# Performance work log

Measured on AMD Instinct MI355X. Metric: run time of the kernel, lower is better.

## Reference

```python
import jax, jax.numpy as jnp
import numpy as np

KEY_DIM = 64
SCALE_PER_SEQ = 1.0 / np.sqrt(KEY_DIM).astype(np.float32)
SCALE_OVER_SEQS = 1.0 / np.sqrt(KEY_DIM).astype(np.float32)


def setup_inputs() -> dict:
    key = jax.random.key(0)
    ks = jax.random.split(key, 6)
    b, i, t, j, d, dv, kd = 4, 512, 32, 256, 512, 512, KEY_DIM
    w_scale = 0.05
    return {
        "input_seq": jax.random.normal(ks[0], (b, i, d), jnp.float32),
        "memory_x": jax.random.normal(ks[1], (b, t, j, d), jnp.float32),
        "memory_y": jax.random.normal(ks[2], (b, t, j, dv), jnp.float32),
        "Wq": jax.random.normal(ks[3], (d, kd), jnp.float32) * w_scale,
        "bq": jnp.zeros((kd,), jnp.float32),
        "Wk": jax.random.normal(ks[4], (d, kd), jnp.float32) * w_scale,
        "bk": jnp.zeros((kd,), jnp.float32),
        "Wv": jax.random.normal(ks[5], (dv, dv), jnp.float32) * w_scale,
        "bv": jnp.zeros((dv,), jnp.float32),
    }


def reference(input_seq, memory_x, memory_y, Wq, bq, Wk, bk, Wv, bv):
    # Projections (Dense layers)
    queries = input_seq @ Wq + bq          # [b, i, kd]
    keys = memory_x @ Wk + bk              # [b, t, j, kd]
    values = memory_y @ Wv + bv            # [b, t, j, dv]

    # Level 1: within-sequence attention
    attn_mat = jnp.einsum('bik,btjk->btij', queries, keys)          # [b, t, i, j]
    per_seq_attn = jax.nn.softmax(SCALE_PER_SEQ * attn_mat, axis=-1)
    per_seq_retrieved = jnp.einsum('btij,btjk->btik', per_seq_attn, values)  # [b, t, i, dv]

    # Level 2: over-sequences attention (max-reduce over j, softmax over t)
    mem_seq_attn = jnp.max(attn_mat, axis=-1)                       # [b, t, i]
    mem_seq_attn = jax.nn.softmax(SCALE_OVER_SEQS * mem_seq_attn, axis=1)

    retrieved = jnp.einsum('bti,btik->bik', mem_seq_attn, per_seq_retrieved)  # [b, i, dv]
    return retrieved
```

## Files before the change

kernel.cpp:

```cpp
#include <hip/hip_runtime.h>
#include <cstdint>

#define B_ 4
#define I_ 512
#define T_ 32
#define J_ 256
#define D_ 512
#define DV_ 512
#define KD_ 64
#define TJ_ (T_*J_)
#define BI_ (B_*I_)
#define MK_ (B_*T_*J_)

typedef unsigned short u16;
typedef __attribute__((ext_vector_type(8))) u16 u16x8;
typedef __attribute__((ext_vector_type(4))) u16 u16x4;
typedef __attribute__((ext_vector_type(8))) short bf16x8;
typedef __attribute__((ext_vector_type(4))) float f32x4;

__device__ __forceinline__ u16 f2bf(float f){
  unsigned u = __float_as_uint(f);
  u += 0x7fffu + ((u >> 16) & 1u);
  return (u16)(u >> 16);
}
__device__ __forceinline__ float bf2f(u16 h){ return __uint_as_float(((unsigned)h) << 16); }

#define GLD16(gsrc, ldst) __builtin_amdgcn_global_load_lds( \
    (const __attribute__((address_space(1))) unsigned int*)(gsrc), \
    (__attribute__((address_space(3))) unsigned int*)(ldst), 16, 0, 0)

__global__ __launch_bounds__(256) void k_prep(const float* __restrict__ Y, u16* __restrict__ Yt,
                                              const float* __restrict__ Wq, const float* __restrict__ Wk,
                                              const float* __restrict__ Wv, u16* __restrict__ wqt,
                                              u16* __restrict__ wkt, u16* __restrict__ wvt){
  __shared__ __align__(16) u16 tileT[64][72];
  int bid = blockIdx.x;
  int tid = threadIdx.x;
  if (bid < 4096){
    int kx = bid & 127, ny = (bid >> 7) & 7, b = bid >> 10;
    int k0 = kx*64, n0 = ny*64;
    #pragma unroll
    for (int s=0;s<4;++s){
      int idx = tid + s*256; int r = idx>>4, c4 = idx&15;
      const float4 v = *(const float4*)&Y[((size_t)b*TJ_ + k0 + r)*DV_ + n0 + c4*4];
      tileT[c4*4+0][r] = f2bf(v.x);
      tileT[c4*4+1][r] = f2bf(v.y);
      tileT[c4*4+2][r] = f2bf(v.z);
      tileT[c4*4+3][r] = f2bf(v.w);
    }
    __syncthreads();
    #pragma unroll
    for (int s=0;s<2;++s){
      int idx = tid + s*256; int rn = idx>>3, c8 = idx&7;
      *(u16x8*)&Yt[((size_t)b*DV_ + n0 + rn)*TJ_ + k0 + c8*8] = *(const u16x8*)&tileT[rn][c8*8];
    }
  } else {
    int gid = (bid - 4096)*256 + tid;
    if (gid < 32768){
      int n = gid >> 9, k = gid & 511;
      wqt[gid] = f2bf(Wq[(size_t)k*64 + n]);
    } else if (gid < 65536){
      int g = gid - 32768;
      int n = g >> 9, k = g & 511;
      wkt[g] = f2bf(Wk[(size_t)k*64 + n]);
    } else {
      int g = gid - 65536;
      int n = g >> 9, k = g & 511;
      wvt[g] = f2bf(Wv[(size_t)k*512 + n]);
    }
  }
}

__global__ __launch_bounds__(256) void k_proj(const float* __restrict__ mx, const float* __restrict__ iseq,
                                              const u16* __restrict__ wkt, const u16* __restrict__ wqt,
                                              const float* __restrict__ bk, const float* __restrict__ bq,
                                              u16* __restrict__ kbf, u16* __restrict__ qbf){
  __shared__ __align__(16) u16 As[32][72];
  __shared__ __align__(16) u16 Bs[64][72];
  int bid = blockIdx.x;
  const float* A; const u16* Bt; const float* bias; u16* C; int row0;
  if (bid < 1024){ A = mx;   Bt = wkt; bias = bk; C = kbf; row0 = bid*32; }
  else           { A = iseq; Bt = wqt; bias = bq; C = qbf; row0 = (bid-1024)*32; }
  int tid = threadIdx.x;
  int lane = tid & 63, wv = tid >> 6;
  int lrow = lane & 15, lk8 = (lane >> 4) * 8;
  int mf = wv >> 1, nfb = (wv & 1) * 2;
  int ar = tid >> 4, ac4 = tid & 15;
  int br = tid >> 3, bc8 = tid & 7;
  f32x4 acc[2];
  acc[0] = (f32x4){0.f,0.f,0.f,0.f}; acc[1] = (f32x4){0.f,0.f,0.f,0.f};

  float4 fa[2][2]; u16x8 fb[2][2];
  #define PROJ_LOAD(pp, k0) { \
    fa[pp][0] = *(const float4*)&A[(size_t)(row0 + ar)*512 + (k0) + ac4*4]; \
    fa[pp][1] = *(const float4*)&A[(size_t)(row0 + ar + 16)*512 + (k0) + ac4*4]; \
    fb[pp][0] = *(const u16x8*)&Bt[(size_t)br*512 + (k0) + bc8*8]; \
    fb[pp][1] = *(const u16x8*)&Bt[(size_t)(br+32)*512 + (k0) + bc8*8]; }

  PROJ_LOAD(0, 0)
  #pragma unroll
  for (int t=0;t<8;++t){
    const int p = t & 1;
    if (t) __syncthreads();
    if (t < 7) PROJ_LOAD(p^1, (t+1)*64)
    #pragma unroll
    for (int s=0;s<2;++s){
      u16x4 o; o[0]=f2bf(fa[p][s].x); o[1]=f2bf(fa[p][s].y); o[2]=f2bf(fa[p][s].z); o[3]=f2bf(fa[p][s].w);
      *(u16x4*)&As[ar + 16*s][ac4*4] = o;
      *(u16x8*)&Bs[br + 32*s][bc8*8] = fb[p][s];
    }
    __syncthreads();
    #pragma unroll
    for (int kk=0;kk<2;++kk){
      bf16x8 a = *(const bf16x8*)&As[mf*16 + lrow][kk*32 + lk8];
      #pragma unroll
      for (int n2=0;n2<2;++n2){
        bf16x8 bb = *(const bf16x8*)&Bs[(nfb+n2)*16 + lrow][kk*32 + lk8];
        acc[n2] = __builtin_amdgcn_mfma_f32_16x16x32_bf16(a, bb, acc[n2], 0, 0, 0);
      }
    }
  }
  #undef PROJ_LOAD
  __syncthreads();
  u16* R = &As[0][0];
  #pragma unroll
  for (int n2=0;n2<2;++n2)
    #pragma unroll
    for (int r=0;r<4;++r){
      int row = mf*16 + (lane>>4)*4 + r;
      int col = (nfb+n2)*16 + lrow;
      R[row*64 + col] = f2bf(acc[n2][r] + bias[col]);
    }
  __syncthreads();
  {
    int row = tid >> 3, c8 = tid & 7;
    *(u16x8*)&C[(size_t)(row0+row)*64 + c8*8] = *(const u16x8*)&R[row*64 + c8*8];
  }
}

__global__ __launch_bounds__(256) void k_score(const u16* __restrict__ Qbf, const u16* __restrict__ Kbf,
                                               u16* __restrict__ P, float* __restrict__ mb, float* __restrict__ zb){
  __shared__ __align__(16) u16 Qs[64][72];
  __shared__ __align__(16) u16 Ks[256][72];
  __shared__ float smax[4][64];
  __shared__ float ssum[4][64];
  __shared__ float mrow[64];
  int tid = threadIdx.x;
  int i0 = blockIdx.x*64, t = blockIdx.y, b = blockIdx.z;
  int lane = tid & 63, wv = tid >> 6;
  int lrow = lane & 15, lk = (lane >> 4) * 8;

  #pragma unroll
  for (int s=0;s<2;++s){
    int idx = tid + s*256; int r = idx>>3, c8 = idx&7;
    *(u16x8*)&Qs[r][c8*8] = *(const u16x8*)&Qbf[((size_t)b*I_ + i0 + r)*KD_ + c8*8];
  }
  #pragma unroll
  for (int s=0;s<8;++s){
    int idx = tid + s*256; int r = idx>>3, c8 = idx&7;
    *(u16x8*)&Ks[r][c8*8] = *(const u16x8*)&Kbf[(((size_t)b*T_ + t)*J_ + r)*KD_ + c8*8];
  }
  __syncthreads();

  f32x4 acc[4][4];
  #pragma unroll
  for (int i=0;i<4;++i)
    #pragma unroll
    for (int j=0;j<4;++j) acc[i][j] = (f32x4){0.f,0.f,0.f,0.f};

  #pragma unroll
  for (int kk=0;kk<2;++kk){
    bf16x8 a[4], bb[4];
    #pragma unroll
    for (int mf=0;mf<4;++mf) a[mf] = *(const bf16x8*)&Qs[mf*16 + lrow][kk*32 + lk];
    #pragma unroll
    for (int nf=0;nf<4;++nf) bb[nf] = *(const bf16x8*)&Ks[wv*64 + nf*16 + lrow][kk*32 + lk];
    #pragma unroll
    for (int mf=0;mf<4;++mf)
      #pragma unroll
      for (int nf=0;nf<4;++nf)
        acc[mf][nf] = __builtin_amdgcn_mfma_f32_16x16x32_bf16(a[mf], bb[nf], acc[mf][nf], 0, 0, 0);
  }

  #pragma unroll
  for (int mf=0;mf<4;++mf)
    #pragma unroll
    for (int r=0;r<4;++r){
      float v = acc[mf][0][r];
      #pragma unroll
      for (int nf=1;nf<4;++nf) v = fmaxf(v, acc[mf][nf][r]);
      v = fmaxf(v, __shfl_xor(v, 1));
      v = fmaxf(v, __shfl_xor(v, 2));
      v = fmaxf(v, __shfl_xor(v, 4));
      v = fmaxf(v, __shfl_xor(v, 8));
      if (lrow == 0) smax[wv][mf*16 + (lane>>4)*4 + r] = v;
    }
  __syncthreads();
  if (tid < 64){
    float m = fmaxf(fmaxf(smax[0][tid], smax[1][tid]), fmaxf(smax[2][tid], smax[3][tid]));
    mrow[tid] = m;
    mb[((size_t)b*T_ + t)*I_ + i0 + tid] = m;
  }
  __syncthreads();

  #pragma unroll
  for (int mf=0;mf<4;++mf)
    #pragma unroll
    for (int r=0;r<4;++r){
      int row = mf*16 + (lane>>4)*4 + r;
      float M = mrow[row];
      float ssm = 0.f;
      #pragma unroll
      for (int nf=0;nf<4;++nf){
        float p = __expf(0.125f*(acc[mf][nf][r] - M));
        acc[mf][nf][r] = p;
        ssm += p;
      }
      ssm += __shfl_xor(ssm, 1);
      ssm += __shfl_xor(ssm, 2);
      ssm += __shfl_xor(ssm, 4);
      ssm += __shfl_xor(ssm, 8);
      if (lrow == 0) ssum[wv][row] = ssm;
    }
  __syncthreads();
  if (tid < 64){
    float z = ssum[0][tid] + ssum[1][tid] + ssum[2][tid] + ssum[3][tid];
    zb[((size_t)b*T_ + t)*I_ + i0 + tid] = z;
  }

  u16* Ps = &Ks[0][0];
  #pragma unroll
  for (int mf=0;mf<4;++mf)
    #pragma unroll
    for (int nf=0;nf<4;++nf)
      #pragma unroll
      for (int r=0;r<4;++r){
        int row = mf*16 + (lane>>4)*4 + r;
        int col = wv*64 + nf*16 + lrow;
        Ps[row*264 + col] = f2bf(acc[mf][nf][r]);
      }
  __syncthreads();
  #pragma unroll
  for (int s=0;s<8;++s){
    int idx = tid + s*256; int r = idx>>5, c8 = idx&31;
    *(u16x8*)&P[(((size_t)b*T_ + t)*I_ + i0 + r)*J_ + c8*8] = *(const u16x8*)&Ps[r*264 + c8*8];
  }
}

template<int CH>
__global__ __launch_bounds__(256,2) void k_passB(const u16* __restrict__ P, const float* __restrict__ mbp,
                                                 const float* __restrict__ zbp, const u16* __restrict__ Yt,
                                                 u16* __restrict__ Up){
  constexpr int TPC = T_/CH;
  constexpr int NS = TPC*4;
  __shared__ __align__(16) u16 Bsh[2][8192];
  __shared__ float cs[TPC][128];
  int tid = threadIdx.x;
  int lane = tid & 63, wv = tid >> 6, wm = wv >> 1, wn = wv & 1;
  int lrow = lane & 15, lg = lane >> 4;

  int NWG = 16*B_*CH;
  int per = NWG >> 3;
  int logical = (blockIdx.x & 7)*per + (blockIdx.x >> 3);
  int group = logical >> 4, within = logical & 15;
  int ix = within & 3, ny = within >> 2;
  int b = group / CH, ch = group % CH;
  int i0 = ix*128, n0 = ny*128;

  int l8 = lane >> 3, sl = lane & 7;

  auto STAGEB = [&](int step, int pp){
    int tt = step >> 2, st = step & 3;
    int t = ch*TPC + tt, j0 = st*64;
    const u16* Ybase = &Yt[((size_t)b*DV_ + n0)*TJ_ + (size_t)t*J_];
    #pragma unroll
    for (int s=0;s<4;++s){
      int row = (wv*4+s)*8 + l8;
      int colA = j0 + ((sl ^ (row & 7)) << 3);
      GLD16(Ybase + (size_t)row*TJ_ + colA, (u16*)Bsh[pp] + (wv*4+s)*512);
    }
  };

  STAGEB(0, 0);

  if (tid < 128){
    int i = i0 + tid;
    float w[T_];
    float lmax = -3.0e38f;
    #pragma unroll
    for (int t=0;t<T_;++t){
      float mt = 0.125f * mbp[((size_t)b*T_ + t)*I_ + i];
      w[t] = mt;
      lmax = fmaxf(lmax, mt);
    }
    float W = 0.f;
    #pragma unroll
    for (int t=0;t<T_;++t){ float e = __expf(w[t] - lmax); w[t] = e; W += e; }
    float inv = 1.f / W;
    #pragma unroll
    for (int tt=0;tt<TPC;++tt)
      cs[tt][tid] = w[ch*TPC+tt] * inv / zbp[((size_t)b*T_ + ch*TPC + tt)*I_ + i];
  }
  __syncthreads();

  f32x4 acc[4][4];
  #pragma unroll
  for (int i=0;i<4;++i)
    #pragma unroll
    for (int j=0;j<4;++j) acc[i][j] = (f32x4){0.f,0.f,0.f,0.f};

  for (int tt = 0; tt < TPC; ++tt){
    if (tt){
      #pragma unroll
      for (int mf=0;mf<4;++mf)
        #pragma unroll
        for (int r=0;r<4;++r){
          int row = wm*64 + mf*16 + lg*4 + r;
          float ratio = cs[tt-1][row] / cs[tt][row];
          #pragma unroll
          for (int nf=0;nf<4;++nf) acc[mf][nf][r] *= ratio;
        }
    }
    int t = ch*TPC + tt;
    const u16* Pbase = &P[(((size_t)b*T_ + t)*I_ + i0)*J_];
    #pragma unroll
    for (int st = 0; st < 4; ++st){
      const int step = tt*4 + st;
      const int pp = step & 1;
      if (step + 1 < NS) STAGEB(step+1, pp^1);
      const u16* Pj = Pbase + st*64;
      #pragma unroll
      for (int kk=0;kk<2;++kk){
        bf16x8 a[4], bb[4];
        #pragma unroll
        for (int mf=0;mf<4;++mf)
          a[mf] = *(const bf16x8*)&Pj[(size_t)(wm*64 + mf*16 + lrow)*J_ + kk*32 + lg*8];
        #pragma unroll
        for (int nf=0;nf<4;++nf){
          int br = wn*64 + nf*16 + lrow;
          int off = br*128 + ((kk*64 + lg*16) ^ ((br & 7) << 4));
          bb[nf] = *(const bf16x8*)((const char*)Bsh[pp] + off);
        }
        #pragma unroll
        for (int mf=0;mf<4;++mf)
          #pragma unroll
          for (int nf=0;nf<4;++nf)
            acc[mf][nf] = __builtin_amdgcn_mfma_f32_16x16x32_bf16(a[mf], bb[nf], acc[mf][nf], 0, 0, 0);
      }
      __syncthreads();
    }
  }

  u16* R = (u16*)&Bsh[0][0];
  #pragma unroll
  for (int mf=0;mf<4;++mf)
    #pragma unroll
    for (int r=0;r<4;++r){
      int row = wm*64 + mf*16 + lg*4 + r;
      float cfin = cs[TPC-1][row];
      #pragma unroll
      for (int nf=0;nf<4;++nf){
        int col = wn*64 + nf*16 + lrow;
        R[row*128 + col] = f2bf(acc[mf][nf][r] * cfin);
      }
    }
  __syncthreads();
  u16* Ub = &Up[(size_t)ch*BI_*DV_ + ((size_t)b*I_ + i0)*DV_ + n0];
  #pragma unroll
  for (int s=0;s<8;++s){
    int id = tid + s*256;
    int row = id >> 4, c8 = id & 15;
    *(u16x8*)&Ub[(size_t)row*DV_ + c8*8] = *(const u16x8*)&R[row*128 + c8*8];
  }
}

template<int CH>
__global__ __launch_bounds__(256) void k_final(const u16* __restrict__ Up, const u16* __restrict__ Bt,
                                               const float* __restrict__ bv, float* __restrict__ out){
  __shared__ __align__(16) u16 As[32][72];
  __shared__ __align__(16) u16 Bs[64][72];
  int tid = threadIdx.x;
  int lane = tid & 63, wv = tid >> 6;
  int lrow = lane & 15, lk8 = (lane >> 4) * 8;
  int bid = blockIdx.x;
  int swz = (bid & 7)*64 + (bid >> 3);
  int row0 = (swz >> 3)*32, col0 = (swz & 7)*64;
  int mf = wv >> 1, nfb = (wv & 1)*2;
  const size_t S = (size_t)BI_*DV_;
  int ar = tid >> 3, ac8 = tid & 7;
  f32x4 acc[2];
  acc[0] = (f32x4){0.f,0.f,0.f,0.f}; acc[1] = (f32x4){0.f,0.f,0.f,0.f};

  u16x8 pa[2][CH]; u16x8 rb[2][2];
  #define FIN_LOAD(pp, k0) { \
    _Pragma("unroll") \
    for (int c=0;c<CH;++c) pa[pp][c] = *(const u16x8*)&Up[(size_t)c*S + (size_t)(row0+ar)*512 + (k0) + ac8*8]; \
    _Pragma("unroll") \
    for (int s=0;s<2;++s) rb[pp][s] = *(const u16x8*)&Bt[(size_t)(col0 + (tid>>3) + 32*s)*512 + (k0) + ac8*8]; }

  FIN_LOAD(0, 0)
  #pragma unroll
  for (int t=0;t<8;++t){
    const int p = t & 1;
    if (t) __syncthreads();
    if (t < 7) FIN_LOAD(p^1, (t+1)*64)
    u16x8 o;
    #pragma unroll
    for (int e=0;e<8;++e){
      float v = 0.f;
      #pragma unroll
      for (int c=0;c<CH;++c) v += bf2f(pa[p][c][e]);
      o[e] = f2bf(v);
    }
    *(u16x8*)&As[ar][ac8*8] = o;
    #pragma unroll
    for (int s=0;s<2;++s) *(u16x8*)&Bs[(tid>>3) + 32*s][ac8*8] = rb[p][s];
    __syncthreads();
    #pragma unroll
    for (int kk=0;kk<2;++kk){
      bf16x8 a = *(const bf16x8*)&As[mf*16 + lrow][kk*32 + lk8];
      #pragma unroll
      for (int n2=0;n2<2;++n2){
        bf16x8 bb = *(const bf16x8*)&Bs[(nfb+n2)*16 + lrow][kk*32 + lk8];
        acc[n2] = __builtin_amdgcn_mfma_f32_16x16x32_bf16(a, bb, acc[n2], 0, 0, 0);
      }
    }
  }
  #undef FIN_LOAD
  #pragma unroll
  for (int n2=0;n2<2;++n2)
    #pragma unroll
    for (int r=0;r<4;++r){
      int row = row0 + mf*16 + (lane>>4)*4 + r;
      int col = col0 + (nfb+n2)*16 + lrow;
      out[(size_t)row*DV_ + col] = acc[n2][r] + bv[col];
    }
}

extern "C" void kernel_launch(void* const* d_in, const int* in_sizes, int n_in,
                              void* d_out, int out_size, void* d_ws, size_t ws_size,
                              hipStream_t stream){
  const float* input_seq = (const float*)d_in[0];
  const float* memory_x  = (const float*)d_in[1];
  const float* memory_y  = (const float*)d_in[2];
  const float* Wq = (const float*)d_in[3];
  const float* bq = (const float*)d_in[4];
  const float* Wk = (const float*)d_in[5];
  const float* bk = (const float*)d_in[6];
  const float* Wv = (const float*)d_in[7];
  const float* bv = (const float*)d_in[8];
  float* out = (float*)d_out;

  char* ws = (char*)d_ws;
  size_t off = 0;
  auto alloc = [&](size_t bytes)->void*{
    void* p = ws + off; off += (bytes + 255) & ~(size_t)255; return p;
  };
  u16*   wqt = (u16*)  alloc((size_t)KD_*D_*2);
  u16*   wkt = (u16*)  alloc((size_t)KD_*D_*2);
  u16*   wvt = (u16*)  alloc((size_t)DV_*DV_*2);
  u16*   qbf = (u16*)  alloc((size_t)BI_*KD_*2);
  u16*   kbf = (u16*)  alloc((size_t)MK_*KD_*2);
  u16*   yt  = (u16*)  alloc((size_t)B_*DV_*TJ_*2);
  u16*   Pb  = (u16*)  alloc((size_t)B_*T_*I_*J_*2);
  float* mb  = (float*)alloc((size_t)B_*T_*I_*4);
  float* zb  = (float*)alloc((size_t)B_*T_*I_*4);
  u16*   Up  = (u16*)  alloc((size_t)8*BI_*DV_*2);

  k_prep<<<4096 + 1280, 256, 0, stream>>>(memory_y, yt, Wq, Wk, Wv, wqt, wkt, wvt);
  k_proj<<<1024 + 64, 256, 0, stream>>>(memory_x, input_seq, wkt, wqt, bk, bq, kbf, qbf);
  k_score<<<dim3(I_/64, T_, B_), 256, 0, stream>>>(qbf, kbf, Pb, mb, zb);
  k_passB<8><<<16*B_*8, 256, 0, stream>>>(Pb, mb, zb, yt, Up);
  k_final<8><<<512, 256, 0, stream>>>(Up, wvt, bv, out);
}
```

Before: 112.4 us.

## Stage P tiles through LDS and halve passB N-tile to raise occupancy

In k_passB the P operand now goes through a swizzled LDS tile instead of being read straight from global memory in the MFMA loop. The output N-tile shrinks from 128 to 64 columns, which doubles the grid and halves the accumulators, and launch bounds rise to 4 blocks per SM. The LDS double buffer is replaced by a single buffer with sync, stage, sync, so loads no longer overlap compute within a block. The intent is better latency hiding from occupancy and coalesced P loads, at the cost of more P re-reads across N-tiles and lost intra-block pipelining.

```diff
diff --git a/kernel.cpp b/kernel.cpp
--- a/kernel.cpp
+++ b/kernel.cpp
@@ -248,40 +248,46 @@
 }
 
 template<int CH>
-__global__ __launch_bounds__(256,2) void k_passB(const u16* __restrict__ P, const float* __restrict__ mbp,
+__global__ __launch_bounds__(256,4) void k_passB(const u16* __restrict__ P, const float* __restrict__ mbp,
                                                  const float* __restrict__ zbp, const u16* __restrict__ Yt,
                                                  u16* __restrict__ Up){
   constexpr int TPC = T_/CH;
   constexpr int NS = TPC*4;
-  __shared__ __align__(16) u16 Bsh[2][8192];
+  __shared__ __align__(16) u16 As[128*64];
+  __shared__ __align__(16) u16 Bs[64*64];
   __shared__ float cs[TPC][128];
   int tid = threadIdx.x;
   int lane = tid & 63, wv = tid >> 6, wm = wv >> 1, wn = wv & 1;
   int lrow = lane & 15, lg = lane >> 4;
 
-  int NWG = 16*B_*CH;
-  int per = NWG >> 3;
-  int logical = (blockIdx.x & 7)*per + (blockIdx.x >> 3);
-  int group = logical >> 4, within = logical & 15;
+  int logical = (blockIdx.x & 7)*128 + (blockIdx.x >> 3);
+  int group = logical >> 5, within = logical & 31;
   int ix = within & 3, ny = within >> 2;
   int b = group / CH, ch = group % CH;
-  int i0 = ix*128, n0 = ny*128;
+  int i0 = ix*128, n0 = ny*64;
 
   int l8 = lane >> 3, sl = lane & 7;
 
-  auto STAGEB = [&](int step, int pp){
+  auto STAGE = [&](int step){
     int tt = step >> 2, st = step & 3;
     int t = ch*TPC + tt, j0 = st*64;
+    const u16* Pbase = &P[(((size_t)b*T_ + t)*I_ + i0)*J_];
     const u16* Ybase = &Yt[((size_t)b*DV_ + n0)*TJ_ + (size_t)t*J_];
     #pragma unroll
     for (int s=0;s<4;++s){
       int row = (wv*4+s)*8 + l8;
       int colA = j0 + ((sl ^ (row & 7)) << 3);
-      GLD16(Ybase + (size_t)row*TJ_ + colA, (u16*)Bsh[pp] + (wv*4+s)*512);
+      GLD16(Pbase + (size_t)row*J_ + colA, (u16*)As + (wv*4+s)*512);
+    }
+    #pragma unroll
+    for (int s=0;s<2;++s){
+      int row = (wv*2+s)*8 + l8;
+      int colA = j0 + ((sl ^ (row & 7)) << 3);
+      GLD16(Ybase + (size_t)row*TJ_ + colA, (u16*)Bs + (wv*2+s)*512);
     }
   };
 
-  STAGEB(0, 0);
+  STAGE(0);
 
   if (tid < 128){
     int i = i0 + tid;
@@ -303,11 +309,11 @@
   }
   __syncthreads();
 
-  f32x4 acc[4][4];
+  f32x4 acc[4][2];
   #pragma unroll
   for (int i=0;i<4;++i)
     #pragma unroll
-    for (int j=0;j<4;++j) acc[i][j] = (f32x4){0.f,0.f,0.f,0.f};
+    for (int j=0;j<2;++j) acc[i][j] = (f32x4){0.f,0.f,0.f,0.f};
 
   for (int tt = 0; tt < TPC; ++tt){
     if (tt){
@@ -318,40 +324,43 @@
           int row = wm*64 + mf*16 + lg*4 + r;
           float ratio = cs[tt-1][row] / cs[tt][row];
           #pragma unroll
-          for (int nf=0;nf<4;++nf) acc[mf][nf][r] *= ratio;
+          for (int nf=0;nf<2;++nf) acc[mf][nf][r] *= ratio;
         }
     }
-    int t = ch*TPC + tt;
-    const u16* Pbase = &P[(((size_t)b*T_ + t)*I_ + i0)*J_];
     #pragma unroll
     for (int st = 0; st < 4; ++st){
       const int step = tt*4 + st;
-      const int pp = step & 1;
-      if (step + 1 < NS) STAGEB(step+1, pp^1);
-      const u16* Pj = Pbase + st*64;
       #pragma unroll
       for (int kk=0;kk<2;++kk){
-        bf16x8 a[4], bb[4];
+        bf16x8 a[4], bb[2];
         #pragma unroll
-        for (int mf=0;mf<4;++mf)
-          a[mf] = *(const bf16x8*)&Pj[(size_t)(wm*64 + mf*16 + lrow)*J_ + kk*32 + lg*8];
+        for (int mf=0;mf<4;++mf){
+          int ar = wm*64 + mf*16 + lrow;
+          int off = ar*128 + ((kk*64 + lg*16) ^ ((ar & 7) << 4));
+          a[mf] = *(const bf16x8*)((const char*)As + off);
+        }
         #pragma unroll
-        for (int nf=0;nf<4;++nf){
-          int br = wn*64 + nf*16 + lrow;
+        for (int nf=0;nf<2;++nf){
+          int br = wn*32 + nf*16 + lrow;
           int off = br*128 + ((kk*64 + lg*16) ^ ((br & 7) << 4));
-          bb[nf] = *(const bf16x8*)((const char*)Bsh[pp] + off);
+          bb[nf] = *(const bf16x8*)((const char*)Bs + off);
         }
         #pragma unroll
         for (int mf=0;mf<4;++mf)
           #pragma unroll
-          for (int nf=0;nf<4;++nf)
+          for (int nf=0;nf<2;++nf)
             acc[mf][nf] = __builtin_amdgcn_mfma_f32_16x16x32_bf16(a[mf], bb[nf], acc[mf][nf], 0, 0, 0);
       }
-      __syncthreads();
-    }
-  }
-
-  u16* R = (u16*)&Bsh[0][0];
+      if (step + 1 < NS){
+        __syncthreads();
+        STAGE(step + 1);
+        __syncthreads();
+      }
+    }
+  }
+
+  __syncthreads();
+  u16* R = (u16*)&As[0];
   #pragma unroll
   for (int mf=0;mf<4;++mf)
     #pragma unroll
@@ -359,18 +368,18 @@
       int row = wm*64 + mf*16 + lg*4 + r;
       float cfin = cs[TPC-1][row];
       #pragma unroll
-      for (int nf=0;nf<4;++nf){
-        int col = wn*64 + nf*16 + lrow;
-        R[row*128 + col] = f2bf(acc[mf][nf][r] * cfin);
+      for (int nf=0;nf<2;++nf){
+        int col = wn*32 + nf*16 + lrow;
+        R[row*64 + col] = f2bf(acc[mf][nf][r] * cfin);
       }
     }
   __syncthreads();
   u16* Ub = &Up[(size_t)ch*BI_*DV_ + ((size_t)b*I_ + i0)*DV_ + n0];
   #pragma unroll
-  for (int s=0;s<8;++s){
+  for (int s=0;s<4;++s){
     int id = tid + s*256;
-    int row = id >> 4, c8 = id & 15;
-    *(u16x8*)&Ub[(size_t)row*DV_ + c8*8] = *(const u16x8*)&R[row*128 + c8*8];
+    int row = id >> 3, c8 = id & 7;
+    *(u16x8*)&Ub[(size_t)row*DV_ + c8*8] = *(const u16x8*)&R[row*64 + c8*8];
   }
 }
 
@@ -470,6 +479,6 @@
   k_prep<<<4096 + 1280, 256, 0, stream>>>(memory_y, yt, Wq, Wk, Wv, wqt, wkt, wvt);
   k_proj<<<1024 + 64, 256, 0, stream>>>(memory_x, input_seq, wkt, wqt, bk, bq, kbf, qbf);
   k_score<<<dim3(I_/64, T_, B_), 256, 0, stream>>>(qbf, kbf, Pb, mb, zb);
-  k_passB<8><<<16*B_*8, 256, 0, stream>>>(Pb, mb, zb, yt, Up);
+  k_passB<8><<<32*B_*8, 256, 0, stream>>>(Pb, mb, zb, yt, Up);
   k_final<8><<<512, 256, 0, stream>>>(Up, wvt, bv, out);
 }
```

New measurement: 96.19 us. 14.4% less time.
